# Kernel optimization log

Hardware: AMD Instinct MI355X
Metric: run time of the kernel (lower is better)

## Reference

```python
import jax, jax.numpy as jnp
import numpy as np

NUM_HEADS = 16
HEAD_DIM = 80
HIDDEN = NUM_HEADS * HEAD_DIM  # 1280
SEQ = 4096
INV_SCALE = 1.0 / np.sqrt(HEAD_DIM)


def setup_inputs() -> dict:
    key = jax.random.key(0)
    ks = jax.random.split(key, 6)
    return {
        "x": jax.random.normal(ks[0], (SEQ, HIDDEN), dtype=jnp.float32),
        "cos_emb": jax.random.uniform(ks[1], (SEQ, HEAD_DIM), dtype=jnp.float32),
        "sin_emb": jax.random.uniform(ks[2], (SEQ, HEAD_DIM), dtype=jnp.float32),
        "w_qkv": jax.random.normal(ks[3], (HIDDEN, 3 * HIDDEN), dtype=jnp.float32) * (1.0 / np.sqrt(HIDDEN)),
        "b_qkv": jnp.zeros((3 * HIDDEN,), dtype=jnp.float32),
        "w_proj": jax.random.normal(ks[4], (HIDDEN, HIDDEN), dtype=jnp.float32) * (1.0 / np.sqrt(HIDDEN)),
        "b_proj": jnp.zeros((HIDDEN,), dtype=jnp.float32),
    }


def _apply_rotary(t, cos_emb, sin_emb):
    # t: (seq, heads, head_dim); cos/sin: (seq, head_dim) -> broadcast over heads
    c = cos_emb[:, None, :]
    s = sin_emb[:, None, :]
    half = HEAD_DIM // 2
    t1, t2 = t[..., :half], t[..., half:]
    rotated = jnp.concatenate([-t2, t1], axis=-1)
    return t * c + rotated * s


def reference(x, cos_emb, sin_emb, w_qkv, b_qkv, w_proj, b_proj):
    seq_len = x.shape[0]
    qkv = x @ w_qkv + b_qkv  # (S, 3*H)
    qkv = qkv.reshape(seq_len, 3, NUM_HEADS, HEAD_DIM)
    q, k, v = qkv[:, 0], qkv[:, 1], qkv[:, 2]  # each (S, nh, hd)
    q = _apply_rotary(q, cos_emb, sin_emb)
    k = _apply_rotary(k, cos_emb, sin_emb)
    # full (non-causal) attention per head; softmax in float32 as in source
    scores = jnp.einsum("ihd,jhd->hij", q, k) * INV_SCALE
    probs = jax.nn.softmax(scores.astype(jnp.float32), axis=-1).astype(x.dtype)
    out = jnp.einsum("hij,jhd->ihd", probs, v)  # (S, nh, hd)
    out = out.reshape(seq_len, HIDDEN)
    return out @ w_proj + b_proj
```

## Files before the change

### kernel.cpp

```cpp
#include <hip/hip_runtime.h>
#include <hip/hip_bf16.h>

#define SEQ 4096
#define HIDDEN 1280
#define NH 16
#define HD 80
#define QKV_N 3840
#define INV_SCALE 0.11180339887498949f
#define LOG2E 1.4426950408889634f

typedef __attribute__((ext_vector_type(8))) short bf16x8;
typedef __attribute__((ext_vector_type(4))) float f32x4;

__device__ __forceinline__ ushort f2bf(float f) {
  union { float f; unsigned u; } v; v.f = f;
  unsigned u = v.u;
  u += 0x7fff + ((u >> 16) & 1);
  return (ushort)(u >> 16);
}
__device__ __forceinline__ float bf2f(ushort h) {
  union { unsigned u; float f; } v; v.u = ((unsigned)h) << 16;
  return v.f;
}
__device__ __forceinline__ unsigned pk_bf16(float a, float b) {
  union { __hip_bfloat162 h; unsigned u; } v;
  v.h = __float22bfloat162_rn(make_float2(a, b));
  return v.u;
}
__device__ __forceinline__ void async16(void* lds, const void* g) {
  __builtin_amdgcn_global_load_lds(
      (const __attribute__((address_space(1))) unsigned*)g,
      (__attribute__((address_space(3))) unsigned*)(unsigned)(size_t)lds,
      16, 0, 0);
}

__global__ __launch_bounds__(256)
void split_rows(const float* __restrict__ A, ushort* __restrict__ hi,
                ushort* __restrict__ lo, int n) {
  int i = (blockIdx.x * 256 + threadIdx.x) * 4;
  if (i >= n) return;
  float4 v = *(const float4*)&A[i];
  ushort h[4], l[4];
  float x[4] = {v.x, v.y, v.z, v.w};
#pragma unroll
  for (int t = 0; t < 4; ++t) {
    h[t] = f2bf(x[t]);
    l[t] = f2bf(x[t] - bf2f(h[t]));
  }
  *(ushort4*)&hi[i] = *(ushort4*)h;
  if (lo) *(ushort4*)&lo[i] = *(ushort4*)l;
}

__global__ __launch_bounds__(256)
void split_T(const float* __restrict__ W, ushort* __restrict__ hiT,
             ushort* __restrict__ loT, int K, int N) {
  __shared__ float T[32][33];
  const int k0 = blockIdx.y * 32, n0 = blockIdx.x * 32;
  for (int e = threadIdx.x; e < 1024; e += 256) {
    int r = e >> 5, c = e & 31;
    T[r][c] = W[(size_t)(k0 + r) * N + n0 + c];
  }
  __syncthreads();
  for (int e = threadIdx.x; e < 1024; e += 256) {
    int r = e >> 5, c = e & 31;
    float x = T[c][r];
    ushort h = f2bf(x);
    size_t idx = (size_t)(n0 + r) * K + k0 + c;
    hiT[idx] = h;
    if (loT) loT[idx] = f2bf(x - bf2f(h));
  }
}

__global__ __launch_bounds__(256, 2)
void gemm_bt_bf16(const ushort* __restrict__ Ab, const ushort* __restrict__ Bb,
                  const float* __restrict__ bias, float* __restrict__ C,
                  int M, int N, int K) {
  __shared__ __align__(16) ushort lds[32768];
  const int tid = threadIdx.x, lane = tid & 63, w = tid >> 6;
  const int m15 = lane & 15, g = lane >> 4;
  const int m0 = blockIdx.y * 128, n0 = blockIdx.x * 128;
  const int wm = (w & 1) * 64, wn = (w >> 1) * 64;

  const ushort* stage_base =
      (w < 2) ? Ab + (size_t)m0 * K + (w & 1) * 32
              : Bb + (size_t)n0 * K + (w & 1) * 32;
  char* ldsb = (char*)lds;

  float bv[4];
#pragma unroll
  for (int ni = 0; ni < 4; ++ni) bv[ni] = bias[n0 + wn + ni * 16 + m15];

  f32x4 acc[4][4];
#pragma unroll
  for (int i = 0; i < 4; ++i)
#pragma unroll
    for (int j = 0; j < 4; ++j) acc[i][j] = (f32x4){0.f, 0.f, 0.f, 0.f};

  const int NK = K >> 6;
#pragma unroll
  for (int i = 0; i < 8; ++i) {
    int o = i * 1024 + lane * 16;
    int row = o >> 6, colb = o & 63;
    async16(ldsb + w * 8192 + o, (const char*)(stage_base + (size_t)row * K) + colb);
  }
  for (int it = 0; it < NK; ++it) {
    const int cur = it & 1;
    const int kn = ((it + 1 < NK) ? it + 1 : it) * 64;
#pragma unroll
    for (int i = 0; i < 8; ++i) {
      int o = i * 1024 + lane * 16;
      int row = o >> 6, colb = o & 63;
      async16(ldsb + (cur ^ 1) * 32768 + w * 8192 + o,
              (const char*)(stage_base + (size_t)row * K + kn) + colb);
    }
    asm volatile("s_waitcnt vmcnt(8)" ::: "memory");
    __builtin_amdgcn_s_barrier();
    __builtin_amdgcn_sched_barrier(0);

    const ushort* L = lds + cur * 16384;
    bf16x8 ah[4][2], bh[4][2];
#pragma unroll
    for (int t = 0; t < 4; ++t) {
      ah[t][0] = *(const bf16x8*)&L[(wm + t * 16 + m15) * 32 + g * 8];
      ah[t][1] = *(const bf16x8*)&L[4096 + (wm + t * 16 + m15) * 32 + g * 8];
      bh[t][0] = *(const bf16x8*)&L[8192 + (wn + t * 16 + m15) * 32 + g * 8];
      bh[t][1] = *(const bf16x8*)&L[12288 + (wn + t * 16 + m15) * 32 + g * 8];
    }
#pragma unroll
    for (int mi = 0; mi < 4; ++mi)
#pragma unroll
      for (int ni = 0; ni < 4; ++ni) {
        acc[mi][ni] = __builtin_amdgcn_mfma_f32_16x16x32_bf16(ah[mi][0], bh[ni][0], acc[mi][ni], 0, 0, 0);
        acc[mi][ni] = __builtin_amdgcn_mfma_f32_16x16x32_bf16(ah[mi][1], bh[ni][1], acc[mi][ni], 0, 0, 0);
      }
    __builtin_amdgcn_s_barrier();
    __builtin_amdgcn_sched_barrier(0);
  }
#pragma unroll
  for (int mi = 0; mi < 4; ++mi)
#pragma unroll
    for (int ni = 0; ni < 4; ++ni) {
      int col = n0 + wn + ni * 16 + m15;
#pragma unroll
      for (int r = 0; r < 4; ++r)
        C[(size_t)(m0 + wm + mi * 16 + g * 4 + r) * N + col] = acc[mi][ni][r] + bv[ni];
    }
}

__global__ __launch_bounds__(256, 2)
void gemm_bt_split(const ushort* __restrict__ Ah, const ushort* __restrict__ Al,
                   const ushort* __restrict__ Bh, const ushort* __restrict__ Bl,
                   const float* __restrict__ bias, float* __restrict__ C,
                   int M, int N, int K) {
  __shared__ __align__(16) ushort lds[32768];
  const int tid = threadIdx.x, lane = tid & 63, w = tid >> 6;
  const int m15 = lane & 15, g = lane >> 4;
  const int m0 = blockIdx.y * 128, n0 = blockIdx.x * 128;
  const int wm = (w & 1) * 64, wn = (w >> 1) * 64;

  const ushort* stage_base =
      (w == 0) ? Ah + (size_t)m0 * K :
      (w == 1) ? Al + (size_t)m0 * K :
      (w == 2) ? Bh + (size_t)n0 * K : Bl + (size_t)n0 * K;
  char* ldsb = (char*)lds;

  float bv[4];
#pragma unroll
  for (int ni = 0; ni < 4; ++ni) bv[ni] = bias[n0 + wn + ni * 16 + m15];

  f32x4 acc[4][4];
#pragma unroll
  for (int i = 0; i < 4; ++i)
#pragma unroll
    for (int j = 0; j < 4; ++j) acc[i][j] = (f32x4){0.f, 0.f, 0.f, 0.f};

  const int NK = K >> 5;
#pragma unroll
  for (int i = 0; i < 8; ++i) {
    int o = i * 1024 + lane * 16;
    int row = o >> 6, colb = o & 63;
    async16(ldsb + w * 8192 + o, (const char*)(stage_base + (size_t)row * K) + colb);
  }
  for (int it = 0; it < NK; ++it) {
    const int cur = it & 1;
    const int kn = ((it + 1 < NK) ? it + 1 : it) * 32;
#pragma unroll
    for (int i = 0; i < 8; ++i) {
      int o = i * 1024 + lane * 16;
      int row = o >> 6, colb = o & 63;
      async16(ldsb + (cur ^ 1) * 32768 + w * 8192 + o,
              (const char*)(stage_base + (size_t)row * K + kn) + colb);
    }
    asm volatile("s_waitcnt vmcnt(8)" ::: "memory");
    __builtin_amdgcn_s_barrier();
    __builtin_amdgcn_sched_barrier(0);

    const ushort* L = lds + cur * 16384;
    bf16x8 ah[4], al[4], bh[4], bl[4];
#pragma unroll
    for (int t = 0; t < 4; ++t) {
      ah[t] = *(const bf16x8*)&L[(wm + t * 16 + m15) * 32 + g * 8];
      al[t] = *(const bf16x8*)&L[4096 + (wm + t * 16 + m15) * 32 + g * 8];
      bh[t] = *(const bf16x8*)&L[8192 + (wn + t * 16 + m15) * 32 + g * 8];
      bl[t] = *(const bf16x8*)&L[12288 + (wn + t * 16 + m15) * 32 + g * 8];
    }
#pragma unroll
    for (int mi = 0; mi < 4; ++mi)
#pragma unroll
      for (int ni = 0; ni < 4; ++ni) {
        acc[mi][ni] = __builtin_amdgcn_mfma_f32_16x16x32_bf16(ah[mi], bh[ni], acc[mi][ni], 0, 0, 0);
        acc[mi][ni] = __builtin_amdgcn_mfma_f32_16x16x32_bf16(ah[mi], bl[ni], acc[mi][ni], 0, 0, 0);
        acc[mi][ni] = __builtin_amdgcn_mfma_f32_16x16x32_bf16(al[mi], bh[ni], acc[mi][ni], 0, 0, 0);
      }
    __builtin_amdgcn_s_barrier();
    __builtin_amdgcn_sched_barrier(0);
  }
#pragma unroll
  for (int mi = 0; mi < 4; ++mi)
#pragma unroll
    for (int ni = 0; ni < 4; ++ni) {
      int col = n0 + wn + ni * 16 + m15;
#pragma unroll
      for (int r = 0; r < 4; ++r)
        C[(size_t)(m0 + wm + mi * 16 + g * 4 + r) * N + col] = acc[mi][ni][r] + bv[ni];
    }
}

__global__ __launch_bounds__(256)
void rotary_qk(const float* __restrict__ qkv, const float* __restrict__ cosb,
               const float* __restrict__ sinb, ushort* __restrict__ Qb,
               ushort* __restrict__ Kb) {
  int id = blockIdx.x * 256 + threadIdx.x;
  int j = id % 48;
  int h = (id / 48) % NH;
  int s = id / (48 * NH);
  size_t qrow = (size_t)((h << 12) + s) * 96;
  if (j < 40) {
    size_t base = (size_t)s * QKV_N + h * HD;
    float c1 = cosb[s * HD + j],      s1 = sinb[s * HD + j];
    float c2 = cosb[s * HD + j + 40], s2 = sinb[s * HD + j + 40];
    const float QS = INV_SCALE * LOG2E;
    float q1 = qkv[base + j], q2 = qkv[base + j + 40];
    Qb[qrow + j]      = f2bf((q1 * c1 - q2 * s1) * QS);
    Qb[qrow + j + 40] = f2bf((q2 * c2 + q1 * s2) * QS);
    float k1 = qkv[base + HIDDEN + j], k2 = qkv[base + HIDDEN + j + 40];
    Kb[qrow + j]      = f2bf(k1 * c1 - k2 * s1);
    Kb[qrow + j + 40] = f2bf(k2 * c2 + k1 * s2);
  } else {
    int d = 80 + (j - 40) * 2;
    Qb[qrow + d] = 0; Qb[qrow + d + 1] = 0;
    Kb[qrow + d] = 0; Kb[qrow + d + 1] = 0;
  }
}

__global__ __launch_bounds__(256)
void v_trans(const float* __restrict__ qkv, ushort* __restrict__ VbT) {
  __shared__ float T[64][81];
  const int h = blockIdx.y, s0 = blockIdx.x * 64;
  for (int e = threadIdx.x; e < 5120; e += 256) {
    int r = e / 80, d = e % 80;
    T[r][d] = qkv[(size_t)(s0 + r) * QKV_N + 2 * HIDDEN + h * HD + d];
  }
  __syncthreads();
  for (int e = threadIdx.x; e < 2560; e += 256) {
    int d = e >> 5, rp = (e & 31) * 2;
    ushort2 p;
    p.x = f2bf(T[rp][d]);
    p.y = f2bf(T[rp + 1][d]);
    *(ushort2*)&VbT[(size_t)h * 80 * SEQ + (size_t)d * SEQ + s0 + rp] = p;
  }
}

#define LPS 88
#define LKS 104
#define LVS 88
__global__ __launch_bounds__(256, 2)
void attn_mfma(const ushort* __restrict__ Qb, const ushort* __restrict__ Kb,
               const ushort* __restrict__ VbT, float* __restrict__ Op,
               float* __restrict__ lp) {
  __shared__ __align__(16) ushort lds[39936];
  ushort* Ps = lds;
  char* ldsb = (char*)lds;

  const int tid = threadIdx.x, lane = tid & 63, w = tid >> 6;
  const int m15 = lane & 15, g = lane >> 4;
  const int h = blockIdx.y, q0 = blockIdx.x * 128, half = blockIdx.z;
  const size_t hq = (size_t)h * SEQ * 96;
  const ushort* Qg = Qb + hq + (size_t)q0 * 96;
  const char* Kg = (const char*)(Kb + hq);
  const ushort* Vg = VbT + (size_t)h * 80 * SEQ;

  bf16x8 qf[2][3];
#pragma unroll
  for (int mi = 0; mi < 2; ++mi)
#pragma unroll
    for (int c = 0; c < 3; ++c)
      qf[mi][c] = *(const bf16x8*)&Qg[(w * 32 + mi * 16 + m15) * 96 + c * 32 + g * 8];

  const char* sbase[7];
  int sstride[7];
#pragma unroll
  for (int i = 0; i < 7; ++i) {
    int c = tid + i * 256;
    if (c < 832) {
      int r = c / 13, cc = c - r * 13;
      sbase[i] = Kg + r * 192 + (cc == 12 ? 176 : cc * 16);
      sstride[i] = 192;
    } else if (c < 1712) {
      int cv = c - 832;
      int r = cv / 11, cc = cv - r * 11;
      sbase[i] = (const char*)(Vg + (size_t)r * SEQ) + (cc >= 8 ? 112 : cc * 16);
      sstride[i] = 2;
    } else {
      sbase[i] = Kg;
      sstride[i] = 192;
    }
  }
  const int dbase = 22528 + tid * 16;

  {
    const size_t kb0 = (size_t)(half * (SEQ / 2));
#pragma unroll
    for (int i = 0; i < 7; ++i)
      async16(ldsb + dbase + i * 4096, sbase[i] + kb0 * sstride[i]);
  }

  f32x4 o_[2][5];
#pragma unroll
  for (int mi = 0; mi < 2; ++mi)
#pragma unroll
    for (int n = 0; n < 5; ++n) o_[mi][n] = (f32x4){0.f, 0.f, 0.f, 0.f};
  float l_part[2] = {0.f, 0.f};

  const int NT = SEQ / 128;
  for (int kt = 0; kt < NT; ++kt) {
    const int cur = kt & 1;
    {
      const size_t kn = (size_t)(half * (SEQ / 2) + ((kt + 1 < NT) ? kt + 1 : kt) * 64);
      const int db = dbase + (cur ^ 1) * 28672;
#pragma unroll
      for (int i = 0; i < 7; ++i)
        async16(ldsb + db + i * 4096, sbase[i] + kn * sstride[i]);
    }
    asm volatile("s_waitcnt vmcnt(7)" ::: "memory");
    __builtin_amdgcn_s_barrier();
    __builtin_amdgcn_sched_barrier(0);

    ushort* Ks = lds + 11264 + cur * 14336;
    ushort* Vt = Ks + 6656;

    f32x4 st[2][4];
#pragma unroll
    for (int mi = 0; mi < 2; ++mi)
#pragma unroll
      for (int j = 0; j < 4; ++j) st[mi][j] = (f32x4){0.f, 0.f, 0.f, 0.f};
#pragma unroll
    for (int j = 0; j < 4; ++j)
#pragma unroll
      for (int c = 0; c < 3; ++c) {
        bf16x8 kf = *(const bf16x8*)&Ks[(j * 16 + m15) * LKS + c * 32 + g * 8];
        st[0][j] = __builtin_amdgcn_mfma_f32_16x16x32_bf16(kf, qf[0][c], st[0][j], 0, 0, 0);
        st[1][j] = __builtin_amdgcn_mfma_f32_16x16x32_bf16(kf, qf[1][c], st[1][j], 0, 0, 0);
      }
#pragma unroll
    for (int mi = 0; mi < 2; ++mi) {
      float ls = 0.f;
#pragma unroll
      for (int j = 0; j < 4; ++j) {
        float p0 = __builtin_amdgcn_exp2f(st[mi][j][0]);
        float p1 = __builtin_amdgcn_exp2f(st[mi][j][1]);
        float p2 = __builtin_amdgcn_exp2f(st[mi][j][2]);
        float p3 = __builtin_amdgcn_exp2f(st[mi][j][3]);
        ls += (p0 + p1) + (p2 + p3);
        uint2 pw;
        pw.x = pk_bf16(p0, p1);
        pw.y = pk_bf16(p2, p3);
        *(uint2*)&Ps[(w * 32 + mi * 16 + m15) * LPS + j * 16 + g * 4] = pw;
      }
      l_part[mi] += ls;
    }
    asm volatile("s_waitcnt lgkmcnt(0)" ::: "memory");
#pragma unroll
    for (int kc = 0; kc < 2; ++kc) {
      bf16x8 pf0 = *(const bf16x8*)&Ps[(w * 32 + m15) * LPS + kc * 32 + g * 8];
      bf16x8 pf1 = *(const bf16x8*)&Ps[(w * 32 + 16 + m15) * LPS + kc * 32 + g * 8];
#pragma unroll
      for (int n = 0; n < 5; ++n) {
        bf16x8 vf = *(const bf16x8*)&Vt[(n * 16 + m15) * LVS + kc * 32 + g * 8];
        o_[0][n] = __builtin_amdgcn_mfma_f32_16x16x32_bf16(pf0, vf, o_[0][n], 0, 0, 0);
        o_[1][n] = __builtin_amdgcn_mfma_f32_16x16x32_bf16(pf1, vf, o_[1][n], 0, 0, 0);
      }
    }
    __builtin_amdgcn_s_barrier();
    __builtin_amdgcn_sched_barrier(0);
  }
  float l_red[2];
#pragma unroll
  for (int mi = 0; mi < 2; ++mi) {
    float t = l_part[mi];
    t += __shfl_xor(t, 16);
    t += __shfl_xor(t, 32);
    l_red[mi] = t;
  }
  if (g == 0) {
    lp[(size_t)half * SEQ * NH + (size_t)(q0 + w * 32 + m15) * NH + h] = l_red[0];
    lp[(size_t)half * SEQ * NH + (size_t)(q0 + w * 32 + 16 + m15) * NH + h] = l_red[1];
  }
  float* Oph = Op + (size_t)half * SEQ * HIDDEN;
#pragma unroll
  for (int mi = 0; mi < 2; ++mi)
#pragma unroll
    for (int r = 0; r < 4; ++r) {
      int grow = q0 + w * 32 + mi * 16 + g * 4 + r;
#pragma unroll
      for (int n = 0; n < 5; ++n)
        Oph[(size_t)grow * HIDDEN + h * HD + n * 16 + m15] = o_[mi][n][r];
    }
}

__global__ __launch_bounds__(256)
void merge_split(const float* __restrict__ Op, const float* __restrict__ lp,
                 ushort* __restrict__ ao_hi, ushort* __restrict__ ao_lo) {
  int id = blockIdx.x * 256 + threadIdx.x;
  int i4 = id * 4;
  int s = i4 / HIDDEN, col = i4 % HIDDEN, hh = col / HD;
  float4 a = *(const float4*)&Op[i4];
  float4 b = *(const float4*)&Op[(size_t)SEQ * HIDDEN + i4];
  float l = lp[s * NH + hh] + lp[SEQ * NH + s * NH + hh];
  float inv = 1.f / l;
  float x[4] = {(a.x + b.x) * inv, (a.y + b.y) * inv,
                (a.z + b.z) * inv, (a.w + b.w) * inv};
  ushort h[4], lo[4];
#pragma unroll
  for (int t = 0; t < 4; ++t) {
    h[t] = f2bf(x[t]);
    lo[t] = f2bf(x[t] - bf2f(h[t]));
  }
  *(ushort4*)&ao_hi[i4] = *(ushort4*)h;
  *(ushort4*)&ao_lo[i4] = *(ushort4*)lo;
}

extern "C" void kernel_launch(void* const* d_in, const int* in_sizes, int n_in,
                              void* d_out, int out_size, void* d_ws, size_t ws_size,
                              hipStream_t stream) {
  const float* x      = (const float*)d_in[0];
  const float* cosb   = (const float*)d_in[1];
  const float* sinb   = (const float*)d_in[2];
  const float* w_qkv  = (const float*)d_in[3];
  const float* b_qkv  = (const float*)d_in[4];
  const float* w_proj = (const float*)d_in[5];
  const float* b_proj = (const float*)d_in[6];
  float* out = (float*)d_out;

  char* ws = (char*)d_ws;
  float*  qkv   = (float*)ws;
  float*  Op    = (float*)ws;
  float*  lp    = (float*)(ws + 41943040);
  ushort* ao_hi = (ushort*)(ws + 42467328);
  ushort* ao_lo = (ushort*)(ws + 52953088);
  size_t o = 62914560;
  ushort* xhi = (ushort*)(ws + o);
  ushort* Qb  = (ushort*)(ws + o);
  o += 20971520;
  ushort* wqT_h = (ushort*)(ws + o);
  ushort* Kb    = (ushort*)(ws + o);
  o += 19660800;
  ushort* VbT   = (ushort*)(ws + o); o += 10485760;
  ushort* wpT_h = (ushort*)(ws + o); o += 3276800;
  ushort* wpT_l = (ushort*)(ws + o);

  split_rows<<<SEQ * HIDDEN / 1024, 256, 0, stream>>>(x, xhi, nullptr, SEQ * HIDDEN);
  split_T<<<dim3(QKV_N / 32, HIDDEN / 32), 256, 0, stream>>>(w_qkv, wqT_h, nullptr, HIDDEN, QKV_N);
  split_T<<<dim3(HIDDEN / 32, HIDDEN / 32), 256, 0, stream>>>(w_proj, wpT_h, wpT_l, HIDDEN, HIDDEN);
  gemm_bt_bf16<<<dim3(QKV_N / 128, SEQ / 128), 256, 0, stream>>>(
      xhi, wqT_h, b_qkv, qkv, SEQ, QKV_N, HIDDEN);
  rotary_qk<<<SEQ * NH * 48 / 256, 256, 0, stream>>>(qkv, cosb, sinb, Qb, Kb);
  v_trans<<<dim3(SEQ / 64, NH), 256, 0, stream>>>(qkv, VbT);
  attn_mfma<<<dim3(SEQ / 128, NH, 2), 256, 0, stream>>>(Qb, Kb, VbT, Op, lp);
  merge_split<<<SEQ * HIDDEN / 1024, 256, 0, stream>>>(Op, lp, ao_hi, ao_lo);
  gemm_bt_split<<<dim3(HIDDEN / 128, SEQ / 128), 256, 0, stream>>>(
      ao_hi, ao_lo, wpT_h, wpT_l, b_proj, out, SEQ, HIDDEN, HIDDEN);
}
```

Measured before the change: 365.8 us.

## Drop split-KV attention, fuse normalization into epilogue, swizzle GEMM block order

The attention kernel now walks the full key sequence per block instead of splitting it into two halves. That removes the partial-output and partial-sum buffers and the separate merge kernel, and normalization plus hi/lo bf16 splitting move into the attention epilogue. Both GEMMs switch to a 1D grid with a block-index swizzle meant to improve L2 reuse. The trade is half as many attention blocks (512 instead of 1024), so occupancy and parallelism on the many-CU device drop, in exchange for less global memory traffic and one fewer launch.

```diff
diff --git a/kernel.cpp b/kernel.cpp
--- a/kernel.cpp
+++ b/kernel.cpp
@@ -78,7 +78,10 @@
   __shared__ __align__(16) ushort lds[32768];
   const int tid = threadIdx.x, lane = tid & 63, w = tid >> 6;
   const int m15 = lane & 15, g = lane >> 4;
-  const int m0 = blockIdx.y * 128, n0 = blockIdx.x * 128;
+  const int id = blockIdx.x;
+  const int swz = (id & 7) * ((int)gridDim.x >> 3) + (id >> 3);
+  const int nbx = N >> 7;
+  const int m0 = (swz / nbx) * 128, n0 = (swz % nbx) * 128;
   const int wm = (w & 1) * 64, wn = (w >> 1) * 64;
 
   const ushort* stage_base =
@@ -155,7 +158,10 @@
   __shared__ __align__(16) ushort lds[32768];
   const int tid = threadIdx.x, lane = tid & 63, w = tid >> 6;
   const int m15 = lane & 15, g = lane >> 4;
-  const int m0 = blockIdx.y * 128, n0 = blockIdx.x * 128;
+  const int id = blockIdx.x;
+  const int swz = (id & 7) * ((int)gridDim.x >> 3) + (id >> 3);
+  const int nbx = N >> 7;
+  const int m0 = (swz / nbx) * 128, n0 = (swz % nbx) * 128;
   const int wm = (w & 1) * 64, wn = (w >> 1) * 64;
 
   const ushort* stage_base =
@@ -276,15 +282,15 @@
 #define LVS 88
 __global__ __launch_bounds__(256, 2)
 void attn_mfma(const ushort* __restrict__ Qb, const ushort* __restrict__ Kb,
-               const ushort* __restrict__ VbT, float* __restrict__ Op,
-               float* __restrict__ lp) {
+               const ushort* __restrict__ VbT, ushort* __restrict__ ao_hi,
+               ushort* __restrict__ ao_lo) {
   __shared__ __align__(16) ushort lds[39936];
   ushort* Ps = lds;
   char* ldsb = (char*)lds;
 
   const int tid = threadIdx.x, lane = tid & 63, w = tid >> 6;
   const int m15 = lane & 15, g = lane >> 4;
-  const int h = blockIdx.y, q0 = blockIdx.x * 128, half = blockIdx.z;
+  const int h = blockIdx.y, q0 = blockIdx.x * 128;
   const size_t hq = (size_t)h * SEQ * 96;
   const ushort* Qg = Qb + hq + (size_t)q0 * 96;
   const char* Kg = (const char*)(Kb + hq);
@@ -318,12 +324,9 @@
   }
   const int dbase = 22528 + tid * 16;
 
-  {
-    const size_t kb0 = (size_t)(half * (SEQ / 2));
-#pragma unroll
-    for (int i = 0; i < 7; ++i)
-      async16(ldsb + dbase + i * 4096, sbase[i] + kb0 * sstride[i]);
-  }
+#pragma unroll
+  for (int i = 0; i < 7; ++i)
+    async16(ldsb + dbase + i * 4096, sbase[i]);
 
   f32x4 o_[2][5];
 #pragma unroll
@@ -332,11 +335,11 @@
     for (int n = 0; n < 5; ++n) o_[mi][n] = (f32x4){0.f, 0.f, 0.f, 0.f};
   float l_part[2] = {0.f, 0.f};
 
-  const int NT = SEQ / 128;
+  const int NT = SEQ / 64;
   for (int kt = 0; kt < NT; ++kt) {
     const int cur = kt & 1;
     {
-      const size_t kn = (size_t)(half * (SEQ / 2) + ((kt + 1 < NT) ? kt + 1 : kt) * 64);
+      const size_t kn = (size_t)(((kt + 1 < NT) ? kt + 1 : kt) * 64);
       const int db = dbase + (cur ^ 1) * 28672;
 #pragma unroll
       for (int i = 0; i < 7; ++i)
@@ -394,50 +397,30 @@
     __builtin_amdgcn_s_barrier();
     __builtin_amdgcn_sched_barrier(0);
   }
-  float l_red[2];
+  float linv[2][4];
 #pragma unroll
   for (int mi = 0; mi < 2; ++mi) {
     float t = l_part[mi];
     t += __shfl_xor(t, 16);
     t += __shfl_xor(t, 32);
-    l_red[mi] = t;
-  }
-  if (g == 0) {
-    lp[(size_t)half * SEQ * NH + (size_t)(q0 + w * 32 + m15) * NH + h] = l_red[0];
-    lp[(size_t)half * SEQ * NH + (size_t)(q0 + w * 32 + 16 + m15) * NH + h] = l_red[1];
-  }
-  float* Oph = Op + (size_t)half * SEQ * HIDDEN;
+#pragma unroll
+    for (int r = 0; r < 4; ++r)
+      linv[mi][r] = 1.f / __shfl(t, g * 4 + r);
+  }
 #pragma unroll
   for (int mi = 0; mi < 2; ++mi)
 #pragma unroll
     for (int r = 0; r < 4; ++r) {
       int grow = q0 + w * 32 + mi * 16 + g * 4 + r;
-#pragma unroll
-      for (int n = 0; n < 5; ++n)
-        Oph[(size_t)grow * HIDDEN + h * HD + n * 16 + m15] = o_[mi][n][r];
-    }
-}
-
-__global__ __launch_bounds__(256)
-void merge_split(const float* __restrict__ Op, const float* __restrict__ lp,
-                 ushort* __restrict__ ao_hi, ushort* __restrict__ ao_lo) {
-  int id = blockIdx.x * 256 + threadIdx.x;
-  int i4 = id * 4;
-  int s = i4 / HIDDEN, col = i4 % HIDDEN, hh = col / HD;
-  float4 a = *(const float4*)&Op[i4];
-  float4 b = *(const float4*)&Op[(size_t)SEQ * HIDDEN + i4];
-  float l = lp[s * NH + hh] + lp[SEQ * NH + s * NH + hh];
-  float inv = 1.f / l;
-  float x[4] = {(a.x + b.x) * inv, (a.y + b.y) * inv,
-                (a.z + b.z) * inv, (a.w + b.w) * inv};
-  ushort h[4], lo[4];
-#pragma unroll
-  for (int t = 0; t < 4; ++t) {
-    h[t] = f2bf(x[t]);
-    lo[t] = f2bf(x[t] - bf2f(h[t]));
-  }
-  *(ushort4*)&ao_hi[i4] = *(ushort4*)h;
-  *(ushort4*)&ao_lo[i4] = *(ushort4*)lo;
+      size_t base = (size_t)grow * HIDDEN + h * HD + m15;
+#pragma unroll
+      for (int n = 0; n < 5; ++n) {
+        float x = o_[mi][n][r] * linv[mi][r];
+        ushort hi = f2bf(x);
+        ao_hi[base + n * 16] = hi;
+        ao_lo[base + n * 16] = f2bf(x - bf2f(hi));
+      }
+    }
 }
 
 extern "C" void kernel_launch(void* const* d_in, const int* in_sizes, int n_in,
@@ -454,8 +437,6 @@
 
   char* ws = (char*)d_ws;
   float*  qkv   = (float*)ws;
-  float*  Op    = (float*)ws;
-  float*  lp    = (float*)(ws + 41943040);
   ushort* ao_hi = (ushort*)(ws + 42467328);
   ushort* ao_lo = (ushort*)(ws + 52953088);
   size_t o = 62914560;
@@ -472,12 +453,11 @@
   split_rows<<<SEQ * HIDDEN / 1024, 256, 0, stream>>>(x, xhi, nullptr, SEQ * HIDDEN);
   split_T<<<dim3(QKV_N / 32, HIDDEN / 32), 256, 0, stream>>>(w_qkv, wqT_h, nullptr, HIDDEN, QKV_N);
   split_T<<<dim3(HIDDEN / 32, HIDDEN / 32), 256, 0, stream>>>(w_proj, wpT_h, wpT_l, HIDDEN, HIDDEN);
-  gemm_bt_bf16<<<dim3(QKV_N / 128, SEQ / 128), 256, 0, stream>>>(
+  gemm_bt_bf16<<<(QKV_N / 128) * (SEQ / 128), 256, 0, stream>>>(
       xhi, wqT_h, b_qkv, qkv, SEQ, QKV_N, HIDDEN);
   rotary_qk<<<SEQ * NH * 48 / 256, 256, 0, stream>>>(qkv, cosb, sinb, Qb, Kb);
   v_trans<<<dim3(SEQ / 64, NH), 256, 0, stream>>>(qkv, VbT);
-  attn_mfma<<<dim3(SEQ / 128, NH, 2), 256, 0, stream>>>(Qb, Kb, VbT, Op, lp);
-  merge_split<<<SEQ * HIDDEN / 1024, 256, 0, stream>>>(Op, lp, ao_hi, ao_lo);
-  gemm_bt_split<<<dim3(HIDDEN / 128, SEQ / 128), 256, 0, stream>>>(
+  attn_mfma<<<dim3(SEQ / 128, NH), 256, 0, stream>>>(Qb, Kb, VbT, ao_hi, ao_lo);
+  gemm_bt_split<<<(HIDDEN / 128) * (SEQ / 128), 256, 0, stream>>>(
       ao_hi, ao_lo, wpT_h, wpT_l, b_proj, out, SEQ, HIDDEN, HIDDEN);
 }
```

Measured after the change: 355.0 us. 3.0% less time.
